# Kernel optimization log

Measured on AMD Instinct MI355X. Metric: run time of the kernel, lower is better.

The kernel has to match this reference:

```python
import jax, jax.numpy as jnp
import numpy as np

M_LOOKBACK = 7          # m: number of previous steps
TAU = 3                 # skip between timesteps
KERNEL_SIZE = M_LOOKBACK + 1   # 8
NUM_KERNELS = 74
C_IN = 7
BATCH = 32
SEQ_LEN = 4096


def setup_inputs() -> dict:
    key = jax.random.key(0)
    k1, k2 = jax.random.split(key)
    x = jax.random.normal(k1, (BATCH, SEQ_LEN, C_IN), dtype=jnp.float32)
    kernels = jax.random.normal(k2, (NUM_KERNELS, KERNEL_SIZE, 3), dtype=jnp.float32)
    return {"x": x, "kernels": kernels}


def reference(x, kernels):
    # x: (B, L, C); kernels: (74, K=8, 3)
    B, L, C = x.shape
    K = KERNEL_SIZE
    idx = jnp.arange(L)[:, None] - jnp.arange(K)[None, :] * TAU          # (L, K)
    valid = (idx >= 0)
    win = jnp.where(valid[None, :, :, None],
                    x[:, jnp.clip(idx, 0), :], 0.0)                      # (B, L, K, C)
    # conv2d with padding=(0,1) along time (width) axis, cross-correlation:
    wp = jnp.pad(win, ((0, 0), (1, 1), (0, 0), (0, 0)))                  # (B, L+2, K, C)
    ws = jnp.stack([wp[:, j:j + L] for j in range(3)], axis=-1)          # (B, L, K, C, 3)
    # First 73 kernels applied to every channel, channel-major stacking order.
    out73 = jnp.einsum('blicj,kij->blck', ws, kernels[:-1])              # (B, L, C, 73)
    out73 = out73.reshape(B, L, C * (NUM_KERNELS - 1))
    # Last kernel applied to one channel (original picks a random channel; use 0).
    out_last = jnp.einsum('blij,ij->bl', ws[:, :, :, 0, :], kernels[-1])[..., None]
    return jnp.concatenate([out73, out_last], axis=-1)                   # (B, L, 512)
```

## Files before the change

### kernel.cpp

```cpp
#include <hip/hip_runtime.h>

#define BATCH    32
#define SEQLEN   4096
#define CIN      7
#define NKERN    74
#define NCOL     512
#define TT       32
#define TG       16
#define NTAP     24
#define HALO     22
#define WROW     25
#define XROW     56

__global__ __launch_bounds__(256) void dilated_convbank_kernel(
    const float* __restrict__ x,
    const float* __restrict__ kern,
    float* __restrict__ out)
{
    __shared__ __align__(16) float Ws[NKERN * WROW];
    __shared__ __align__(16) float xs[CIN * XROW];

    const int tid = threadIdx.x;
    const int t0  = blockIdx.x * TT;
    const int b   = blockIdx.y;

    for (int idx = tid; idx < NKERN * NTAP; idx += 256) {
        const int k = idx / NTAP, m = idx - k * NTAP;
        const int i = 7 - m / 3, j = m % 3;
        Ws[k * WROW + m] = kern[(k * 8 + i) * 3 + j];
    }
    for (int idx = tid; idx < CIN * XROW; idx += 256) {
        const int c = idx / XROW, tl = idx - c * XROW;
        const int t = t0 - HALO + tl;
        float v = 0.f;
        if (t >= 0 && t < SEQLEN)
            v = x[(b * SEQLEN + t) * CIN + c];
        xs[c * XROW + tl] = v;
    }
    __syncthreads();

    const bool lastTile = (t0 + TT == SEQLEN);

    #pragma unroll
    for (int cc = 0; cc < 2; ++cc) {
        const int q = tid + cc * 256;
        int c, k;
        if (q == NCOL - 1) { c = 0; k = NKERN - 1; }
        else               { c = q / 73; k = q - c * 73; }

        float W[NTAP];
        #pragma unroll
        for (int m = 0; m < NTAP; ++m) W[m] = Ws[k * WROW + m];
        const float* xrow = &xs[c * XROW];

        float* ob = out + ((size_t)b * SEQLEN + t0) * NCOL + q;

        #pragma unroll
        for (int g = 0; g < TT / TG; ++g) {
            float xw[TG + NTAP];
            #pragma unroll
            for (int v = 0; v < (TG + NTAP) / 4; ++v) {
                const float4 f = ((const float4*)(xrow + g * TG))[v];
                xw[v * 4 + 0] = f.x; xw[v * 4 + 1] = f.y;
                xw[v * 4 + 2] = f.z; xw[v * 4 + 3] = f.w;
            }
            float acc[TG];
            #pragma unroll
            for (int tt = 0; tt < TG; ++tt) acc[tt] = 0.f;
            #pragma unroll
            for (int m = 0; m < NTAP; ++m) {
                const float w = W[m];
                #pragma unroll
                for (int tt = 0; tt < TG; ++tt)
                    acc[tt] += w * xw[tt + m];
            }
            if (lastTile && g == TT / TG - 1) {
                #pragma unroll
                for (int m = 2; m < 23; m += 3)
                    acc[TG - 1] -= W[m] * xw[TG - 1 + m];
            }
            #pragma unroll
            for (int tt = 0; tt < TG; ++tt)
                ob[(size_t)(g * TG + tt) * NCOL] = acc[tt];
        }
    }
}

extern "C" void kernel_launch(void* const* d_in, const int* in_sizes, int n_in,
                              void* d_out, int out_size, void* d_ws, size_t ws_size,
                              hipStream_t stream) {
    const float* x    = (const float*)d_in[0];
    const float* kern = (const float*)d_in[1];
    float* out = (float*)d_out;

    dim3 grid(SEQLEN / TT, BATCH);
    dilated_convbank_kernel<<<grid, 256, 0, stream>>>(x, kern, out);
}
```

Baseline: 270.1 us.

## Stage outputs in shared memory for float4 stores and halve time tile

Output tiles are now written to a 32KB shared buffer and then copied to global memory with coalesced float4 stores, replacing per-thread strided scalar stores. The time tile drops from 32 to 16 steps, which doubles the grid, and the shared weight table is removed so each thread reads its 24 taps straight from global memory. The cc loop is no longer unrolled. The shared staging buffer lowers occupancy, and the halo overhead per output grows.

```diff
diff --git a/kernel.cpp b/kernel.cpp
--- a/kernel.cpp
+++ b/kernel.cpp
@@ -5,30 +5,23 @@
 #define CIN      7
 #define NKERN    74
 #define NCOL     512
-#define TT       32
-#define TG       16
+#define TT       16
 #define NTAP     24
 #define HALO     22
-#define WROW     25
-#define XROW     56
+#define XROW     40
 
 __global__ __launch_bounds__(256) void dilated_convbank_kernel(
     const float* __restrict__ x,
     const float* __restrict__ kern,
     float* __restrict__ out)
 {
-    __shared__ __align__(16) float Ws[NKERN * WROW];
     __shared__ __align__(16) float xs[CIN * XROW];
+    __shared__ __align__(16) float Ot[TT * NCOL];
 
     const int tid = threadIdx.x;
     const int t0  = blockIdx.x * TT;
     const int b   = blockIdx.y;
 
-    for (int idx = tid; idx < NKERN * NTAP; idx += 256) {
-        const int k = idx / NTAP, m = idx - k * NTAP;
-        const int i = 7 - m / 3, j = m % 3;
-        Ws[k * WROW + m] = kern[(k * 8 + i) * 3 + j];
-    }
     for (int idx = tid; idx < CIN * XROW; idx += 256) {
         const int c = idx / XROW, tl = idx - c * XROW;
         const int t = t0 - HALO + tl;
@@ -41,7 +34,7 @@
 
     const bool lastTile = (t0 + TT == SEQLEN);
 
-    #pragma unroll
+    #pragma unroll 1
     for (int cc = 0; cc < 2; ++cc) {
         const int q = tid + cc * 256;
         int c, k;
@@ -50,40 +43,47 @@
 
         float W[NTAP];
         #pragma unroll
-        for (int m = 0; m < NTAP; ++m) W[m] = Ws[k * WROW + m];
+        for (int m = 0; m < NTAP; ++m) {
+            const int i = 7 - m / 3, j = m % 3;
+            W[m] = kern[(k * 8 + i) * 3 + j];
+        }
+
         const float* xrow = &xs[c * XROW];
+        float xw[XROW];
+        #pragma unroll
+        for (int v = 0; v < XROW / 4; ++v) {
+            const float4 f = ((const float4*)xrow)[v];
+            xw[4 * v + 0] = f.x; xw[4 * v + 1] = f.y;
+            xw[4 * v + 2] = f.z; xw[4 * v + 3] = f.w;
+        }
 
-        float* ob = out + ((size_t)b * SEQLEN + t0) * NCOL + q;
+        float acc[TT];
+        #pragma unroll
+        for (int tt = 0; tt < TT; ++tt) acc[tt] = 0.f;
+        #pragma unroll
+        for (int m = 0; m < NTAP; ++m) {
+            const float w = W[m];
+            #pragma unroll
+            for (int tt = 0; tt < TT; ++tt)
+                acc[tt] += w * xw[tt + m];
+        }
+        if (lastTile) {
+            #pragma unroll
+            for (int m = 2; m < 23; m += 3)
+                acc[TT - 1] -= W[m] * xw[TT - 1 + m];
+        }
 
         #pragma unroll
-        for (int g = 0; g < TT / TG; ++g) {
-            float xw[TG + NTAP];
-            #pragma unroll
-            for (int v = 0; v < (TG + NTAP) / 4; ++v) {
-                const float4 f = ((const float4*)(xrow + g * TG))[v];
-                xw[v * 4 + 0] = f.x; xw[v * 4 + 1] = f.y;
-                xw[v * 4 + 2] = f.z; xw[v * 4 + 3] = f.w;
-            }
-            float acc[TG];
-            #pragma unroll
-            for (int tt = 0; tt < TG; ++tt) acc[tt] = 0.f;
-            #pragma unroll
-            for (int m = 0; m < NTAP; ++m) {
-                const float w = W[m];
-                #pragma unroll
-                for (int tt = 0; tt < TG; ++tt)
-                    acc[tt] += w * xw[tt + m];
-            }
-            if (lastTile && g == TT / TG - 1) {
-                #pragma unroll
-                for (int m = 2; m < 23; m += 3)
-                    acc[TG - 1] -= W[m] * xw[TG - 1 + m];
-            }
-            #pragma unroll
-            for (int tt = 0; tt < TG; ++tt)
-                ob[(size_t)(g * TG + tt) * NCOL] = acc[tt];
-        }
+        for (int tt = 0; tt < TT; ++tt)
+            Ot[tt * NCOL + q] = acc[tt];
     }
+    __syncthreads();
+
+    const float4* s4 = (const float4*)Ot;
+    float4* o4 = (float4*)(out + ((size_t)b * SEQLEN + t0) * NCOL);
+    #pragma unroll
+    for (int i = 0; i < (TT * NCOL) / 4 / 256; ++i)
+        o4[tid + i * 256] = s4[tid + i * 256];
 }
 
 extern "C" void kernel_launch(void* const* d_in, const int* in_sizes, int n_in,
```

Measured after the change: 285.1 us. 5.6% more time.
